# Performance work log

Hardware: AMD Instinct MI355X
Metric: run time of the kernel (lower is better)

The kernel has to match this reference:

```python
import jax, jax.numpy as jnp
from jax import lax
import numpy as np

LOG2PI = float(np.log(2.0 * np.pi))
FMIN = float(np.finfo(np.float32).min)


def seq_mask(lengths, maxlen):
    # [B, maxlen] float32
    return (jnp.arange(maxlen)[None] < lengths[:, None]).astype(jnp.float32)


def monotonic_alignment_search(ll, attnmask):
    """Faithful port of GlowTTS.monotonic_alignment_search.
    ll, attnmask: [B, T, S] float32. Returns [B, T, S] float32.
    Note: replicates the source exactly, including stacking backtracked rows
    in descending-j (append) order before masking, as written in the TF code.
    """
    B, T, S = ll.shape
    x_range = jnp.arange(S)[None]  # [1, S]

    def fwd(prob, j_and_ll):
        j, ll_j = j_and_ll  # ll_j: [B, S]
        prev = jnp.pad(prob, ((0, 0), (1, 0)), constant_values=-jnp.inf)[:, :-1]
        max_mask = prob >= prev                       # [B, S] bool
        prob_max = jnp.where(max_mask, prob, prev)
        prob_new = jnp.where(x_range <= j, prob_max + ll_j, FMIN)
        return prob_new, max_mask

    _, direction = lax.scan(fwd, jnp.zeros((B, S), jnp.float32),
                            (jnp.arange(T), jnp.transpose(ll, (1, 0, 2))))
    direction = jnp.transpose(direction, (1, 0, 2)).astype(jnp.int32)  # [B, T, S]
    direction = jnp.where(attnmask.astype(bool), direction, 1)

    index = attnmask[:, 0].sum(axis=-1).astype(jnp.int32) - 1  # [B]
    brange = jnp.arange(B)

    def bwd(index, j):
        attn_j = jax.nn.one_hot(index, S, dtype=jnp.float32)  # drops index<0 like scatter_nd
        d = direction[brange, j, index]                       # [B]
        return index + d - 1, attn_j

    _, attn = lax.scan(bwd, index, jnp.arange(T)[::-1])
    attn = jnp.transpose(attn, (1, 0, 2))  # [B, T, S], rows in append order
    return attn * attnmask


def setup_inputs() -> dict:
    key = jax.random.key(0)
    k1, k2, k3, k4, k5 = jax.random.split(key, 5)
    B, T, S, C = 32, 1200, 384, 160
    latent = jax.random.normal(k1, (B, T, C), dtype=jnp.float32)
    mean = jax.random.normal(k2, (B, S, C), dtype=jnp.float32)
    logdur = jax.random.normal(k3, (B, S), dtype=jnp.float32)
    textlen = jax.random.randint(k4, (B,), S // 2, S + 1).astype(jnp.int32)
    mellen = jax.random.randint(k5, (B,), T // 2, T + 1).astype(jnp.int32)
    return {"latent": latent, "mean": mean, "logdur": logdur,
            "textlen": textlen, "mellen": mellen}


def reference(latent, mean, logdur, textlen, mellen):
    B, T, C = latent.shape
    S = mean.shape[1]
    mask = seq_mask(textlen, S)     # [B, S]
    melmask = seq_mask(mellen, T)   # [B, T]
    attnmask = melmask[..., None] * mask[:, None]  # [B, T, S]

    # pairwise squared distance (cdist via matmul + reduce_sum)
    dist = (jnp.sum(jnp.square(latent), axis=-1, keepdims=True)
            - 2.0 * jnp.einsum('btc,bsc->bts', latent, mean)
            + jnp.sum(jnp.square(mean), axis=-1)[:, None])
    ll = -0.5 * (LOG2PI + dist) * attnmask

    attn = lax.stop_gradient(monotonic_alignment_search(ll, attnmask))
    aligned = jnp.einsum('bts,bsc->btc', attn, mean)  # [B, T, C]

    # negative log-likelihood (dlogdet of the flow omitted: constant here)
    nll = 0.5 * (LOG2PI + jnp.sum(jnp.square(latent - aligned), axis=(1, 2)))
    nll = jnp.mean(nll / (mellen * C).astype(jnp.float32))

    gtdur = jnp.log(jnp.maximum(jnp.sum(attn, axis=1), 1e-05)) * mask
    durloss = jnp.sum(jnp.square(logdur - gtdur), axis=-1) / mellen.astype(jnp.float32)
    durloss = jnp.mean(durloss)

    loss = nll + durloss
    return loss, attn
```

## Files before the change

kernel.cpp:

```cpp
#include <hip/hip_runtime.h>
#include <math.h>

#define LOG2PI 1.8378770664093453f
#define F32MIN (-3.4028234663852886e38f)
#define SMAX 384
#define RST 388
#define NW 38

__global__ __launch_bounds__(64) void k_sums(
    const float* __restrict__ latent, const float* __restrict__ mean,
    float* __restrict__ lx2, float* __restrict__ lm2, int BT, int BS, int C) {
  int row = blockIdx.x;
  int lane = threadIdx.x;
  const float* src;
  float* dst;
  if (row < BT) { src = latent + (size_t)row * C; dst = lx2 + row; }
  else          { src = mean + (size_t)(row - BT) * C; dst = lm2 + (row - BT); }
  float s = 0.f;
  for (int c = lane; c < C; c += 64) { float v = src[c]; s += v * v; }
  #pragma unroll
  for (int off = 32; off; off >>= 1) s += __shfl_down(s, off);
  if (lane == 0) *dst = s;
}

__global__ __launch_bounds__(256) void k_scores(
    const float* __restrict__ latent, const float* __restrict__ mean,
    const float* __restrict__ lx2, const float* __restrict__ lm2,
    const int* __restrict__ textlen, const int* __restrict__ mellen,
    float* __restrict__ ll, int T, int S, int C) {
  int b  = blockIdx.z;
  int t0 = blockIdx.x * 64;
  int s0 = blockIdx.y * 64;
  int mel = mellen[b], txt = textlen[b];
  int tid = threadIdx.x;
  int ty = tid >> 4, tx = tid & 15;
  float* out = ll + ((size_t)b * T + t0) * S + s0;

  if (t0 >= mel || s0 >= txt) {
    float4 z = make_float4(0.f, 0.f, 0.f, 0.f);
    #pragma unroll
    for (int i = 0; i < 4; ++i) {
      int tl = ty * 4 + i;
      if (t0 + tl < T) *(float4*)(out + (size_t)tl * S + tx * 4) = z;
    }
    return;
  }

  __shared__ float At[16][64];
  __shared__ float Bt[16][64];
  float acc[4][4] = {};

  const float* Ab = latent + ((size_t)b * T + t0) * C;
  const float* Bb = mean + ((size_t)b * S + s0) * C;

  for (int kk = 0; kk < C; kk += 16) {
    int r  = tid >> 2;
    int cg = tid & 3;
    float4 a = (t0 + r < T) ? *(const float4*)(Ab + (size_t)r * C + kk + cg * 4)
                            : make_float4(0.f, 0.f, 0.f, 0.f);
    float4 bm = *(const float4*)(Bb + (size_t)r * C + kk + cg * 4);
    At[cg * 4 + 0][r] = a.x;  At[cg * 4 + 1][r] = a.y;
    At[cg * 4 + 2][r] = a.z;  At[cg * 4 + 3][r] = a.w;
    Bt[cg * 4 + 0][r] = bm.x; Bt[cg * 4 + 1][r] = bm.y;
    Bt[cg * 4 + 2][r] = bm.z; Bt[cg * 4 + 3][r] = bm.w;
    __syncthreads();
    #pragma unroll
    for (int k = 0; k < 16; ++k) {
      float4 a4 = *(const float4*)&At[k][ty * 4];
      float4 b4 = *(const float4*)&Bt[k][tx * 4];
      float av[4] = {a4.x, a4.y, a4.z, a4.w};
      float bv[4] = {b4.x, b4.y, b4.z, b4.w};
      #pragma unroll
      for (int i = 0; i < 4; ++i)
        #pragma unroll
        for (int j = 0; j < 4; ++j)
          acc[i][j] = fmaf(av[i], bv[j], acc[i][j]);
    }
    __syncthreads();
  }

  #pragma unroll
  for (int i = 0; i < 4; ++i) {
    int t = t0 + ty * 4 + i;
    if (t >= T) continue;
    float lx = lx2[(size_t)b * T + t];
    float4 o;
    float* po = &o.x;
    #pragma unroll
    for (int j = 0; j < 4; ++j) {
      int s = s0 + tx * 4 + j;
      float d = lx - 2.f * acc[i][j] + lm2[(size_t)b * S + s];
      float v = -0.5f * (LOG2PI + d);
      po[j] = (t < mel && s < txt) ? v : 0.f;
    }
    *(float4*)(out + (size_t)(ty * 4 + i) * S + tx * 4) = o;
  }
}

__device__ __forceinline__ float dpp_shr1_neginf(float x) {
  int r = __builtin_amdgcn_update_dpp(
      __float_as_int(-INFINITY), __float_as_int(x),
      0x138 , 0xf, 0xf, false);
  return __int_as_float(r);
}

template <bool MASKED>
__device__ __forceinline__ void mas_step(
    int t, int sbase, int r, const float2 A0, const float2 A1, const float2 A2,
    float& p0, float& p1, float& p2, float& p3, float& p4, float& p5,
    unsigned& n0, unsigned& n1, unsigned& n2, unsigned& n3, unsigned& n4,
    unsigned& n5) {
  float l0 = A0.x, l1 = A0.y, l2 = A1.x, l3 = A1.y, l4 = A2.x, l5 = A2.y;
  float pm1 = dpp_shr1_neginf(p5);
  unsigned s0b = __float_as_uint(p0 - pm1) >> 31;
  unsigned s1b = __float_as_uint(p1 - p0)  >> 31;
  unsigned s2b = __float_as_uint(p2 - p1)  >> 31;
  unsigned s3b = __float_as_uint(p3 - p2)  >> 31;
  unsigned s4b = __float_as_uint(p4 - p3)  >> 31;
  unsigned s5b = __float_as_uint(p5 - p4)  >> 31;
  n0 |= s0b << r; n1 |= s1b << r; n2 |= s2b << r;
  n3 |= s3b << r; n4 |= s4b << r; n5 |= s5b << r;
  float v0 = fmaxf(p0, pm1) + l0;
  float v1 = fmaxf(p1, p0) + l1;
  float v2 = fmaxf(p2, p1) + l2;
  float v3 = fmaxf(p3, p2) + l3;
  float v4 = fmaxf(p4, p3) + l4;
  float v5 = fmaxf(p5, p4) + l5;
  if (MASKED) {
    p0 = (sbase + 0 <= t) ? v0 : F32MIN;
    p1 = (sbase + 1 <= t) ? v1 : F32MIN;
    p2 = (sbase + 2 <= t) ? v2 : F32MIN;
    p3 = (sbase + 3 <= t) ? v3 : F32MIN;
    p4 = (sbase + 4 <= t) ? v4 : F32MIN;
    p5 = (sbase + 5 <= t) ? v5 : F32MIN;
  } else {
    p0 = v0; p1 = v1; p2 = v2; p3 = v3; p4 = v4; p5 = v5;
  }
}

template <bool MASKED, int ROWS>
__device__ __forceinline__ void scan_chunk_lds(
    const float* __restrict__ rcur, int t0, int sbase,
    float& p0, float& p1, float& p2, float& p3, float& p4, float& p5,
    unsigned* __restrict__ dirT, int cw) {
  unsigned n0 = 0, n1 = 0, n2 = 0, n3 = 0, n4 = 0, n5 = 0;
  const float2* q = (const float2*)(rcur + sbase);
  float2 A0 = q[0 * (RST / 2)], A1 = q[0 * (RST / 2) + 1], A2 = q[0 * (RST / 2) + 2];
  float2 B0 = q[1 * (RST / 2)], B1 = q[1 * (RST / 2) + 1], B2 = q[1 * (RST / 2) + 2];
  float2 C0 = q[2 * (RST / 2)], C1 = q[2 * (RST / 2) + 1], C2 = q[2 * (RST / 2) + 2];
  float2 D0 = q[3 * (RST / 2)], D1 = q[3 * (RST / 2) + 1], D2 = q[3 * (RST / 2) + 2];
  #pragma unroll 1
  for (int r = 0; r < ROWS; r += 4) {
    mas_step<MASKED>(t0 + r, sbase, r, A0, A1, A2,
                     p0, p1, p2, p3, p4, p5, n0, n1, n2, n3, n4, n5);
    {
      int rn = (r + 4 < ROWS) ? r + 4 : ROWS - 1;
      const float2* p = q + (size_t)rn * (RST / 2);
      A0 = p[0]; A1 = p[1]; A2 = p[2];
    }
    mas_step<MASKED>(t0 + r + 1, sbase, r + 1, B0, B1, B2,
                     p0, p1, p2, p3, p4, p5, n0, n1, n2, n3, n4, n5);
    {
      int rn = (r + 5 < ROWS) ? r + 5 : ROWS - 1;
      const float2* p = q + (size_t)rn * (RST / 2);
      B0 = p[0]; B1 = p[1]; B2 = p[2];
    }
    mas_step<MASKED>(t0 + r + 2, sbase, r + 2, C0, C1, C2,
                     p0, p1, p2, p3, p4, p5, n0, n1, n2, n3, n4, n5);
    {
      int rn = (r + 6 < ROWS) ? r + 6 : ROWS - 1;
      const float2* p = q + (size_t)rn * (RST / 2);
      C0 = p[0]; C1 = p[1]; C2 = p[2];
    }
    mas_step<MASKED>(t0 + r + 3, sbase, r + 3, D0, D1, D2,
                     p0, p1, p2, p3, p4, p5, n0, n1, n2, n3, n4, n5);
    {
      int rn = (r + 7 < ROWS) ? r + 7 : ROWS - 1;
      const float2* p = q + (size_t)rn * (RST / 2);
      D0 = p[0]; D1 = p[1]; D2 = p[2];
    }
  }
  unsigned* dcol = dirT + (unsigned)sbase * NW + cw;
  dcol[0] = ~n0; dcol[NW] = ~n1; dcol[2 * NW] = ~n2;
  dcol[3 * NW] = ~n3; dcol[4 * NW] = ~n4; dcol[5 * NW] = ~n5;
}

__global__ __launch_bounds__(256, 1) void k_scan(
    const float* __restrict__ ll, const int* __restrict__ textlen,
    const int* __restrict__ mellen, int* __restrict__ pathidx, int T, int S) {
  int b = blockIdx.x;
  int tid = threadIdx.x;
  int lane = tid & 63;
  __shared__ float rows[2][32][RST];
  __shared__ unsigned dirT[SMAX * NW];

  const float* llb = ll + (size_t)b * T * S;
  int mel = mellen[b], txt = textlen[b];
  int sbase = lane * 6;
  int nfull = T / 32;
  int nch = (T + 31) / 32;
  float p0 = 0.f, p1 = 0.f, p2 = 0.f, p3 = 0.f, p4 = 0.f, p5 = 0.f;

  if (tid >= 64) {
    int lid = tid - 64;
    const float4* g = (const float4*)llb;
    #pragma unroll
    for (int k = 0; k < 16; ++k) {
      int f = k * 192 + lid;
      ((float4*)&rows[0][f / 96][0])[f % 96] = g[f];
    }
  }
  __syncthreads();

  for (int c = 0; c < nch; ++c) {
    if (tid >= 64) {
      int nxt = c + 1;
      if (nxt < nch) {
        int lid = tid - 64;
        const float4* g = (const float4*)(llb + (size_t)nxt * 32 * S);
        if (nxt < nfull) {
          float4 stg[16];
          #pragma unroll
          for (int k = 0; k < 16; ++k) stg[k] = g[k * 192 + lid];
          #pragma unroll
          for (int k = 0; k < 16; ++k) {
            int f = k * 192 + lid;
            ((float4*)&rows[nxt & 1][f / 96][0])[f % 96] = stg[k];
          }
        } else {
          float4 stg[8];
          #pragma unroll
          for (int k = 0; k < 8; ++k) stg[k] = g[k * 192 + lid];
          #pragma unroll
          for (int k = 0; k < 8; ++k) {
            int f = k * 192 + lid;
            ((float4*)&rows[nxt & 1][f / 96][0])[f % 96] = stg[k];
          }
        }
      }
    } else {
      const float* rc = &rows[c & 1][0][0];
      int t0 = c * 32;
      if (c < nfull) {
        if (t0 < S)
          scan_chunk_lds<true, 32>(rc, t0, sbase, p0, p1, p2, p3, p4, p5, dirT, c);
        else
          scan_chunk_lds<false, 32>(rc, t0, sbase, p0, p1, p2, p3, p4, p5, dirT, c);
      } else {
        scan_chunk_lds<false, 16>(rc, t0, sbase, p0, p1, p2, p3, p4, p5, dirT, c);
      }
    }
    __syncthreads();
  }

  if (tid >= 64) return;

  size_t base = (size_t)b * T;
  int k0 = T - mel;
  for (int k = lane; k < k0; k += 64) pathidx[base + k] = txt - 1;

  if (lane == 0) {
    int i = txt - 1;
    int j = mel - 1;
    unsigned w = ~0u;
    bool reload = true;
    for (int k = k0; k < T; ++k) {
      pathidx[base + k] = i;
      if (reload) {
        int ii = (i < 0) ? i + S : i;
        ii = (ii < 0) ? 0 : ii;
        w = (ii < txt) ? dirT[ii * NW + (j >> 5)] : ~0u;
      }
      int d = (int)((w >> (j & 31)) & 1u);
      reload = (d == 0) | ((j & 31) == 0);
      i += d - 1;
      --j;
    }
  }
}

__global__ __launch_bounds__(256) void k_scatter(
    float* __restrict__ attn, const int* __restrict__ pathidx,
    const int* __restrict__ textlen, const int* __restrict__ mellen,
    int B, int T, int S) {
  size_t idx = ((size_t)blockIdx.x * blockDim.x + threadIdx.x) * 4;
  size_t total = (size_t)B * T * S;
  if (idx >= total) return;
  int s = (int)(idx % S);
  size_t row = idx / S;
  int b = (int)(row / T);
  int k = (int)(row % T);
  int pi = pathidx[row];
  int mel = mellen[b], txt = textlen[b];
  float4 o = make_float4(0.f, 0.f, 0.f, 0.f);
  if (k < mel && pi >= 0 && pi < S && pi < txt && pi >= s && pi < s + 4)
    (&o.x)[pi - s] = 1.f;
  *(float4*)(attn + idx) = o;
}

__global__ __launch_bounds__(256) void k_rowloss(
    const float* __restrict__ latent, const float* __restrict__ mean,
    const int* __restrict__ pathidx, const int* __restrict__ textlen,
    const int* __restrict__ mellen, float* __restrict__ rowsum,
    int T, int S, int C) {
  int row = blockIdx.x * 4 + (threadIdx.x >> 6);
  int lane = threadIdx.x & 63;
  int b = row / T, k = row % T;
  int pi = pathidx[row];
  int mel = mellen[b], txt = textlen[b];
  bool on = (k < mel) && (pi >= 0) && (pi < S) && (pi < txt);
  const float* L = latent + (size_t)row * C;
  const float* M = mean + ((size_t)b * S + (on ? pi : 0)) * C;
  float s = 0.f;
  for (int c = lane; c < C; c += 64) {
    float d = L[c] - (on ? M[c] : 0.f);
    s += d * d;
  }
  #pragma unroll
  for (int off = 32; off; off >>= 1) s += __shfl_down(s, off);
  if (lane == 0) rowsum[row] = s;
}

__global__ __launch_bounds__(256) void k_batch(
    const float* __restrict__ rowsum, const int* __restrict__ pathidx,
    const float* __restrict__ logdur, const int* __restrict__ textlen,
    const int* __restrict__ mellen, float* __restrict__ nllc,
    float* __restrict__ durc, int T, int S, int C) {
  int b = blockIdx.x;
  int tid = threadIdx.x;
  __shared__ int hist[512];
  __shared__ float red[256];
  int mel = mellen[b], txt = textlen[b];
  for (int s = tid; s < S; s += 256) hist[s] = 0;
  __syncthreads();
  for (int k = tid; k < T; k += 256) {
    int pi = pathidx[(size_t)b * T + k];
    if (k < mel && pi >= 0 && pi < S && pi < txt) atomicAdd(&hist[pi], 1);
  }
  __syncthreads();
  float part = 0.f;
  for (int s = tid; s < S; s += 256) {
    float cnt = (float)hist[s];
    float gt = logf(fmaxf(cnt, 1e-5f));
    gt = (s < txt) ? gt : 0.f;
    float d = logdur[(size_t)b * S + s] - gt;
    part += d * d;
  }
  red[tid] = part; __syncthreads();
  #pragma unroll
  for (int off = 128; off; off >>= 1) {
    if (tid < off) red[tid] += red[tid + off];
    __syncthreads();
  }
  if (tid == 0) durc[b] = red[0] / (float)mel;
  __syncthreads();
  part = 0.f;
  for (int k = tid; k < T; k += 256) part += rowsum[(size_t)b * T + k];
  red[tid] = part; __syncthreads();
  #pragma unroll
  for (int off = 128; off; off >>= 1) {
    if (tid < off) red[tid] += red[tid + off];
    __syncthreads();
  }
  if (tid == 0) nllc[b] = 0.5f * (LOG2PI + red[0]) / ((float)mel * (float)C);
}

__global__ __launch_bounds__(64) void k_final(
    const float* __restrict__ nllc, const float* __restrict__ durc,
    float* __restrict__ out, int B) {
  int lane = threadIdx.x;
  float v = (lane < B) ? (nllc[lane] + durc[lane]) : 0.f;
  #pragma unroll
  for (int off = 32; off; off >>= 1) v += __shfl_down(v, off);
  if (lane == 0) out[0] = v / (float)B;
}

extern "C" void kernel_launch(void* const* d_in, const int* in_sizes, int n_in,
                              void* d_out, int out_size, void* d_ws, size_t ws_size,
                              hipStream_t stream) {
  (void)n_in; (void)out_size; (void)ws_size;
  const float* latent = (const float*)d_in[0];
  const float* mean   = (const float*)d_in[1];
  const float* logdur = (const float*)d_in[2];
  const int*   textlen = (const int*)d_in[3];
  const int*   mellen  = (const int*)d_in[4];

  int B = in_sizes[3];
  int S = in_sizes[2] / B;
  int C = in_sizes[1] / (B * S);
  int T = in_sizes[0] / (B * C);

  float* out = (float*)d_out;
  float* ll = out + 1;

  char* ws = (char*)d_ws;
  float* lx2    = (float*)ws;
  float* lm2    = lx2 + (size_t)B * T;
  int*   pathidx = (int*)(lm2 + (size_t)B * S);
  float* rowsum  = (float*)(pathidx + (size_t)B * T);
  float* nllc    = rowsum + (size_t)B * T;
  float* durc    = nllc + B;

  k_sums<<<B * T + B * S, 64, 0, stream>>>(latent, mean, lx2, lm2, B * T, B * S, C);

  dim3 g2((T + 63) / 64, (S + 63) / 64, B);
  k_scores<<<g2, 256, 0, stream>>>(latent, mean, lx2, lm2, textlen, mellen, ll, T, S, C);

  k_scan<<<B, 256, 0, stream>>>(ll, textlen, mellen, pathidx, T, S);

  size_t total = (size_t)B * T * S;
  k_scatter<<<(int)((total / 4 + 255) / 256), 256, 0, stream>>>(ll, pathidx, textlen, mellen, B, T, S);

  k_rowloss<<<(B * T) / 4, 256, 0, stream>>>(latent, mean, pathidx, textlen, mellen, rowsum, T, S, C);

  k_batch<<<B, 256, 0, stream>>>(rowsum, pathidx, logdur, textlen, mellen, nllc, durc, T, S, C);

  k_final<<<1, 64, 0, stream>>>(nllc, durc, out, B);
}
```

Before: 347.4 us.

## Skip masked score tiles and stop the alignment scan at each mel length

The scores kernel now returns early for tiles fully outside the text or mel length, or entirely above the diagonal, instead of writing zeros. The scan kernel stops its forward loop after the chunks covering each batch's mel length. It also applies the masked step variant by a fixed chunk index. The LDS row prefetch in the inner scan loop is cut from four rows ahead to two, which lowers register pressure but leaves less latency hidden. Skipped ll entries stay uninitialized, so correctness relies on them never feeding the backtracked path.

```diff
diff --git a/kernel.cpp b/kernel.cpp
--- a/kernel.cpp
+++ b/kernel.cpp
@@ -36,15 +36,7 @@
   int ty = tid >> 4, tx = tid & 15;
   float* out = ll + ((size_t)b * T + t0) * S + s0;
 
-  if (t0 >= mel || s0 >= txt) {
-    float4 z = make_float4(0.f, 0.f, 0.f, 0.f);
-    #pragma unroll
-    for (int i = 0; i < 4; ++i) {
-      int tl = ty * 4 + i;
-      if (t0 + tl < T) *(float4*)(out + (size_t)tl * S + tx * 4) = z;
-    }
-    return;
-  }
+  if (t0 >= mel || s0 >= txt || s0 > t0 + 63) return;
 
   __shared__ float At[16][64];
   __shared__ float Bt[16][64];
@@ -145,40 +137,18 @@
     unsigned* __restrict__ dirT, int cw) {
   unsigned n0 = 0, n1 = 0, n2 = 0, n3 = 0, n4 = 0, n5 = 0;
   const float2* q = (const float2*)(rcur + sbase);
-  float2 A0 = q[0 * (RST / 2)], A1 = q[0 * (RST / 2) + 1], A2 = q[0 * (RST / 2) + 2];
-  float2 B0 = q[1 * (RST / 2)], B1 = q[1 * (RST / 2) + 1], B2 = q[1 * (RST / 2) + 2];
-  float2 C0 = q[2 * (RST / 2)], C1 = q[2 * (RST / 2) + 1], C2 = q[2 * (RST / 2) + 2];
-  float2 D0 = q[3 * (RST / 2)], D1 = q[3 * (RST / 2) + 1], D2 = q[3 * (RST / 2) + 2];
+  float2 A0 = q[0], A1 = q[1], A2 = q[2];
   #pragma unroll 1
-  for (int r = 0; r < ROWS; r += 4) {
+  for (int r = 0; r < ROWS; r += 2) {
+    const float2* qb = q + (size_t)(r + 1) * (RST / 2);
+    float2 B0 = qb[0], B1 = qb[1], B2 = qb[2];
     mas_step<MASKED>(t0 + r, sbase, r, A0, A1, A2,
                      p0, p1, p2, p3, p4, p5, n0, n1, n2, n3, n4, n5);
-    {
-      int rn = (r + 4 < ROWS) ? r + 4 : ROWS - 1;
-      const float2* p = q + (size_t)rn * (RST / 2);
-      A0 = p[0]; A1 = p[1]; A2 = p[2];
-    }
+    int rn = (r + 2 < ROWS) ? (r + 2) : (ROWS - 1);
+    const float2* qa = q + (size_t)rn * (RST / 2);
+    A0 = qa[0]; A1 = qa[1]; A2 = qa[2];
     mas_step<MASKED>(t0 + r + 1, sbase, r + 1, B0, B1, B2,
                      p0, p1, p2, p3, p4, p5, n0, n1, n2, n3, n4, n5);
-    {
-      int rn = (r + 5 < ROWS) ? r + 5 : ROWS - 1;
-      const float2* p = q + (size_t)rn * (RST / 2);
-      B0 = p[0]; B1 = p[1]; B2 = p[2];
-    }
-    mas_step<MASKED>(t0 + r + 2, sbase, r + 2, C0, C1, C2,
-                     p0, p1, p2, p3, p4, p5, n0, n1, n2, n3, n4, n5);
-    {
-      int rn = (r + 6 < ROWS) ? r + 6 : ROWS - 1;
-      const float2* p = q + (size_t)rn * (RST / 2);
-      C0 = p[0]; C1 = p[1]; C2 = p[2];
-    }
-    mas_step<MASKED>(t0 + r + 3, sbase, r + 3, D0, D1, D2,
-                     p0, p1, p2, p3, p4, p5, n0, n1, n2, n3, n4, n5);
-    {
-      int rn = (r + 7 < ROWS) ? r + 7 : ROWS - 1;
-      const float2* p = q + (size_t)rn * (RST / 2);
-      D0 = p[0]; D1 = p[1]; D2 = p[2];
-    }
   }
   unsigned* dcol = dirT + (unsigned)sbase * NW + cw;
   dcol[0] = ~n0; dcol[NW] = ~n1; dcol[2 * NW] = ~n2;
@@ -199,6 +169,8 @@
   int sbase = lane * 6;
   int nfull = T / 32;
   int nch = (T + 31) / 32;
+  int nchb = (mel + 31) / 32;
+  if (nchb > nch) nchb = nch;
   float p0 = 0.f, p1 = 0.f, p2 = 0.f, p3 = 0.f, p4 = 0.f, p5 = 0.f;
 
   if (tid >= 64) {
@@ -212,10 +184,10 @@
   }
   __syncthreads();
 
-  for (int c = 0; c < nch; ++c) {
+  for (int c = 0; c < nchb; ++c) {
     if (tid >= 64) {
       int nxt = c + 1;
-      if (nxt < nch) {
+      if (nxt < nchb) {
         int lid = tid - 64;
         const float4* g = (const float4*)(llb + (size_t)nxt * 32 * S);
         if (nxt < nfull) {
@@ -241,14 +213,12 @@
     } else {
       const float* rc = &rows[c & 1][0][0];
       int t0 = c * 32;
-      if (c < nfull) {
-        if (t0 < S)
-          scan_chunk_lds<true, 32>(rc, t0, sbase, p0, p1, p2, p3, p4, p5, dirT, c);
-        else
-          scan_chunk_lds<false, 32>(rc, t0, sbase, p0, p1, p2, p3, p4, p5, dirT, c);
-      } else {
+      if (c < 12)
+        scan_chunk_lds<true, 32>(rc, t0, sbase, p0, p1, p2, p3, p4, p5, dirT, c);
+      else if (c < nfull)
+        scan_chunk_lds<false, 32>(rc, t0, sbase, p0, p1, p2, p3, p4, p5, dirT, c);
+      else
         scan_chunk_lds<false, 16>(rc, t0, sbase, p0, p1, p2, p3, p4, p5, dirT, c);
-      }
     }
     __syncthreads();
   }
```

Measured after the change: 321.1 us. 1.08x faster.
